# Performance work log

Measured on AMD Instinct MI355X. Metric: run time of the kernel, lower is better.

The kernel has to match this reference:

```python
import jax, jax.numpy as jnp
import numpy as np

B, N, C = 16, 2048, 80
CONF_THR = 0.2
NMS_THR = 0.45
OFFSET = 10000.0  # > max box coordinate, separates classes for batched per-class NMS


def setup_inputs() -> dict:
    key = jax.random.key(0)
    k1, k2, k3, k4 = jax.random.split(key, 4)
    cxcy = jax.random.uniform(k1, (B, N, 2)) * 640.0
    wh = jax.random.uniform(k2, (B, N, 2)) * 100.0 + 1.0
    boxes = jnp.concatenate([cxcy - wh / 2, cxcy + wh / 2], axis=-1)  # (x1,y1,x2,y2)
    scores = jax.random.uniform(k3, (B, N, 1))
    classprobs = jax.random.uniform(k4, (B, N, C))
    detection = jnp.concatenate([boxes, scores, classprobs], axis=-1)  # [B,N,85]
    return {"detection": detection}


def _iou_matrix(boxes):
    # boxes: [N,4] -> [N,N] pairwise IoU (torchvision convention, no +1)
    x1, y1, x2, y2 = boxes[:, 0], boxes[:, 1], boxes[:, 2], boxes[:, 3]
    area = jnp.clip(x2 - x1, 0.0) * jnp.clip(y2 - y1, 0.0)
    ix1 = jnp.maximum(x1[:, None], x1[None, :])
    iy1 = jnp.maximum(y1[:, None], y1[None, :])
    ix2 = jnp.minimum(x2[:, None], x2[None, :])
    iy2 = jnp.minimum(y2[:, None], y2[None, :])
    inter = jnp.clip(ix2 - ix1, 0.0) * jnp.clip(iy2 - iy1, 0.0)
    return inter / (area[:, None] + area[None, :] - inter + 1e-7)


def _filter_image(boxes, scores, classprobs, labels):
    # Confidence filter (target_class=None path)
    cand = scores > CONF_THR
    # Sort by descending score, non-candidates last (sort key is non-differentiable)
    sort_key = jnp.where(cand, scores, -jnp.inf)
    order = jnp.argsort(-jax.lax.stop_gradient(sort_key))
    b = boxes[order]
    s = scores[order]
    cp = classprobs[order]
    lb = labels[order]
    cd = cand[order]
    # Per-class NMS via coordinate offset: boxes of different classes never overlap
    ob = b + lb[:, None].astype(b.dtype) * OFFSET
    iou = _iou_matrix(ob)  # [N,N]
    idx = jnp.arange(N)

    def step(active, i):
        keep_i = active[i]
        active = active & ~(keep_i & (iou[i] > NMS_THR) & (idx > i))
        return active, keep_i

    _, keep = jax.lax.scan(step, cd, idx)
    # Final sort by descending score among kept boxes (max_predictions_per_image=-1)
    final_key = jnp.where(keep, jax.lax.stop_gradient(s), -jnp.inf)
    perm = jnp.argsort(-final_key)
    keep_p = keep[perm]
    m = keep_p.astype(b.dtype)
    out_boxes = b[perm] * m[:, None]
    out_scores = s[perm] * m
    out_classprobs = cp[perm] * m
    out_labels = jnp.where(keep_p, lb[perm], 0)
    return out_boxes, out_scores, out_classprobs, out_labels, keep_p


def reference(detection):
    # split_detections
    boxes = detection[..., :4]
    scores = detection[..., 4]
    cp_all = detection[..., 5:]
    classprobs = jnp.max(cp_all, axis=-1)
    labels = jnp.argmax(cp_all, axis=-1)
    ob, osc, ocp, olb, mask = jax.vmap(_filter_image)(boxes, scores, classprobs, labels)
    # Pack float outputs: [B, N, 6] = boxes(4) + score(1) + classprob(1); padded rows are zero
    out = jnp.concatenate([ob, osc[..., None], ocp[..., None]], axis=-1)
    return out, olb, mask
```

## Files before the change

kernel.cpp:

```cpp
#include <hip/hip_runtime.h>

#define BATCH 16
#define NBOX  2048
#define NCLS  80
#define ROWF  85
#define CONF_THRF 0.2f
#define CONF_BITS 0x3E4CCCCDu
#define NMS_THRF  0.45f
#define CAP   128
#define KCAP  128
#define JOBS  (BATCH*NCLS)

#define WS_SL   0
#define WS_CP   (WS_SL + BATCH*NBOX*8)
#define WS_KC   (WS_CP + BATCH*NBOX*4)
#define WS_KCLS (WS_KC + (size_t)JOBS*KCAP*8)

static __device__ inline unsigned long long shflx64(unsigned long long v, int m) {
  int lo = __shfl_xor((int)(unsigned)(v & 0xffffffffull), m, 64);
  int hi = __shfl_xor((int)(unsigned)(v >> 32), m, 64);
  return ((unsigned long long)(unsigned)hi << 32) | (unsigned)lo;
}

__global__ __launch_bounds__(256) void prep_kernel(const float* __restrict__ det,
                                                   unsigned long long* __restrict__ sl,
                                                   float* __restrict__ cp_ws,
                                                   float* __restrict__ outz) {
  const int tid = threadIdx.x;
  const int lane = tid & 63, wavei = tid >> 6;
  const int sub = lane & 15, grp = lane >> 4;
  const int row = blockIdx.x * 16 + wavei * 4 + grp;

  int gid = blockIdx.x * 256 + tid;
  if (gid < (BATCH * NBOX * 8) / 4)
    ((float4*)outz)[gid] = make_float4(0.f, 0.f, 0.f, 0.f);

  const float* r = det + (size_t)row * ROWF;
  float best = r[5 + sub];
  int bc = sub;
#pragma unroll
  for (int k = 1; k < 5; ++k) {
    float v = r[5 + sub + 16 * k];
    if (v > best) { best = v; bc = sub + 16 * k; }
  }
#pragma unroll
  for (int d = 1; d < 16; d <<= 1) {
    float ov = __shfl_xor(best, d, 16);
    int oc = __shfl_xor(bc, d, 16);
    if (ov > best || (ov == best && oc < bc)) { best = ov; bc = oc; }
  }
  if (sub == 0) {
    sl[row] = ((unsigned long long)__float_as_uint(r[4]) << 32) | (unsigned)bc;
    cp_ws[row] = best;
  }
}

__global__ __launch_bounds__(256) void nms16_kernel(const float* __restrict__ det,
                                                    const unsigned long long* __restrict__ sl,
                                                    unsigned long long* __restrict__ keptc,
                                                    int* __restrict__ kcls) {
  __shared__ unsigned short cand[4][CAP];
  const int tid = threadIdx.x;
  const int lane = tid & 63, wid = tid >> 6;
  const int j = blockIdx.x * 4 + wid;
  const int img = j / NCLS, c = j - img * NCLS;
  const size_t ibase = (size_t)img * NBOX;
  const unsigned long long* slImg = sl + ibase;
  unsigned short* mycand = cand[wid];

  unsigned mymask = 0;
#pragma unroll
  for (int it = 0; it < 32; ++it) {
    unsigned long long v = slImg[it * 64 + lane];
    bool match = ((unsigned)(v >> 32) > CONF_BITS) && ((unsigned)v == (unsigned)c);
    mymask |= (match ? 1u : 0u) << it;
  }
  int mycnt = __popc(mymask);
  int inc = mycnt;
#pragma unroll
  for (int d = 1; d < 64; d <<= 1) { int u = __shfl_up(inc, d, 64); if (lane >= d) inc += u; }
  int mybase = inc - mycnt;
  int total = __shfl(inc, 63, 64);
  int m = total < CAP ? total : CAP;
  {
    unsigned mk = mymask;
    int pos = mybase;
    while (mk) {
      int it = __ffs(mk) - 1; mk &= mk - 1;
      if (pos < CAP) mycand[pos] = (unsigned short)(it * 64 + lane);
      pos++;
    }
  }

  unsigned long long e0 = ~0ull, e1 = ~0ull;
  if (lane < m) {
    int n = mycand[lane];
    e0 = ((unsigned long long)(~(unsigned)(slImg[n] >> 32)) << 32) | (unsigned)n;
  }
  if (lane + 64 < m) {
    int n = mycand[lane + 64];
    e1 = ((unsigned long long)(~(unsigned)(slImg[n] >> 32)) << 32) | (unsigned)n;
  }
  const bool two = (m > 64);
  if (!two) {
#pragma unroll
    for (int k = 2; k <= 64; k <<= 1)
      for (int jj = k >> 1; jj > 0; jj >>= 1) {
        bool amLow = (lane & jj) == 0;
        bool up = ((lane & k) == 0);
        unsigned long long o = shflx64(e0, jj);
        e0 = (up == amLow) ? (e0 < o ? e0 : o) : (e0 > o ? e0 : o);
      }
  } else {
#pragma unroll
    for (int k = 2; k <= 128; k <<= 1)
      for (int jj = k >> 1; jj > 0; jj >>= 1) {
        if (jj == 64) {
          bool up = ((lane & k) == 0);
          if (up ? (e0 > e1) : (e0 < e1)) { unsigned long long t = e0; e0 = e1; e1 = t; }
        } else {
          bool amLow = (lane & jj) == 0;
          bool up0 = ((lane & k) == 0), up1 = (((lane + 64) & k) == 0);
          unsigned long long o0 = shflx64(e0, jj), o1 = shflx64(e1, jj);
          e0 = (up0 == amLow) ? (e0 < o0 ? e0 : o0) : (e0 > o0 ? e0 : o0);
          e1 = (up1 == amLow) ? (e1 < o1 ? e1 : o1) : (e1 > o1 ? e1 : o1);
        }
      }
  }

  const float off = (float)c * 10000.0f;
  bool valid0 = lane < m, valid1 = two && (lane + 64 < m);
  int n0 = (int)((unsigned)e0 & (NBOX - 1));
  int n1 = (int)((unsigned)e1 & (NBOX - 1));
  float x1 = 0, y1 = 0, x2 = 0, y2 = 0, ar = 0;
  if (valid0) {
    const float* rr = det + (ibase + n0) * ROWF;
    x1 = rr[0] + off; y1 = rr[1] + off; x2 = rr[2] + off; y2 = rr[3] + off;
    ar = fmaxf(x2 - x1, 0.0f) * fmaxf(y2 - y1, 0.0f);
  }
  float X1 = 0, Y1 = 0, X2 = 0, Y2 = 0, AR = 0;
  if (valid1) {
    const float* rr = det + (ibase + n1) * ROWF;
    X1 = rr[0] + off; Y1 = rr[1] + off; X2 = rr[2] + off; Y2 = rr[3] + off;
    AR = fmaxf(X2 - X1, 0.0f) * fmaxf(Y2 - Y1, 0.0f);
  }

  unsigned long long keptm0 = 0, und = __ballot(valid0);
  while (und) {
    int i = __ffsll((long long)und) - 1;
    keptm0 |= 1ull << i;
    float kx1 = __shfl(x1, i, 64), ky1 = __shfl(y1, i, 64);
    float kx2 = __shfl(x2, i, 64), ky2 = __shfl(y2, i, 64);
    float kar = __shfl(ar, i, 64);
    float iw = fminf(x2, kx2) - fmaxf(x1, kx1);
    float ih = fminf(y2, ky2) - fmaxf(y1, ky1);
    float inter = fmaxf(iw, 0.0f) * fmaxf(ih, 0.0f);
    float iou = inter / (((kar + ar) - inter) + 1e-7f);
    bool sup = (lane > i) && (iou > NMS_THRF);
    und &= ~__ballot(sup);
    und &= ~(1ull << i);
  }
  unsigned long long keptm1 = 0;
  if (two) {
    bool dead = false;
    unsigned long long km = keptm0;
    while (km) {
      int t = __ffsll((long long)km) - 1; km &= km - 1;
      float kx1 = __shfl(x1, t, 64), ky1 = __shfl(y1, t, 64);
      float kx2 = __shfl(x2, t, 64), ky2 = __shfl(y2, t, 64);
      float kar = __shfl(ar, t, 64);
      float iw = fminf(X2, kx2) - fmaxf(X1, kx1);
      float ih = fminf(Y2, ky2) - fmaxf(Y1, ky1);
      float inter = fmaxf(iw, 0.0f) * fmaxf(ih, 0.0f);
      float iou = inter / (((kar + AR) - inter) + 1e-7f);
      dead |= (iou > NMS_THRF);
    }
    unsigned long long und1 = __ballot(valid1 && !dead);
    while (und1) {
      int i = __ffsll((long long)und1) - 1;
      keptm1 |= 1ull << i;
      float kx1 = __shfl(X1, i, 64), ky1 = __shfl(Y1, i, 64);
      float kx2 = __shfl(X2, i, 64), ky2 = __shfl(Y2, i, 64);
      float kar = __shfl(AR, i, 64);
      float iw = fminf(X2, kx2) - fmaxf(X1, kx1);
      float ih = fminf(Y2, ky2) - fmaxf(Y1, ky1);
      float inter = fmaxf(iw, 0.0f) * fmaxf(ih, 0.0f);
      float iou = inter / (((kar + AR) - inter) + 1e-7f);
      bool sup = (lane > i) && (iou > NMS_THRF);
      und1 &= ~__ballot(sup);
      und1 &= ~(1ull << i);
    }
  }

  unsigned long long* dst = keptc + (size_t)j * KCAP;
  if ((keptm0 >> lane) & 1) {
    int rank = __popcll(keptm0 & ((1ull << lane) - 1ull));
    dst[rank] = (e0 & 0xffffffff00000000ull) | (unsigned)((n0 << 7) | c);
  }
  if (two && ((keptm1 >> lane) & 1)) {
    int rank = __popcll(keptm0) + __popcll(keptm1 & ((1ull << lane) - 1ull));
    dst[rank] = (e1 & 0xffffffff00000000ull) | (unsigned)((n1 << 7) | c);
  }
  if (lane == 0) kcls[j] = __popcll(keptm0) + __popcll(keptm1);
}

__global__ __launch_bounds__(1024) void outr_kernel(const float* __restrict__ det,
                                                    const float* __restrict__ cp_ws,
                                                    const unsigned long long* __restrict__ keptc,
                                                    const int* __restrict__ kcls,
                                                    float* __restrict__ out) {
  __shared__ unsigned long long keys[NBOX];
  __shared__ int offL[NCLS], cntL[NCLS];
  __shared__ int KtotS;
  const int img = blockIdx.x >> 5, seg = blockIdx.x & 31;
  const int tid = threadIdx.x;
  const int lane = tid & 63, wid = tid >> 6;
  const size_t ibase = (size_t)img * NBOX;

  if (wid == 0) {
    int v0 = kcls[img * NCLS + lane];
    int v1 = (lane < NCLS - 64) ? kcls[img * NCLS + 64 + lane] : 0;
    int s0 = v0;
#pragma unroll
    for (int d = 1; d < 64; d <<= 1) { int u = __shfl_up(s0, d, 64); if (lane >= d) s0 += u; }
    int total0 = __shfl(s0, 63, 64);
    int s1 = v1;
#pragma unroll
    for (int d = 1; d < 16; d <<= 1) { int u = __shfl_up(s1, d, 64); if (lane >= d) s1 += u; }
    offL[lane] = s0 - v0; cntL[lane] = v0;
    if (lane < NCLS - 64) { offL[64 + lane] = total0 + s1 - v1; cntL[64 + lane] = v1; }
    if (lane == 15) KtotS = total0 + s1;
  }
  __syncthreads();
  const int K = KtotS;
  if (seg * 64 >= K) return;

  for (int c = wid; c < NCLS; c += 16) {
    int kc = cntL[c], o = offL[c];
    const unsigned long long* src = keptc + (size_t)(img * NCLS + c) * KCAP;
    for (int q = lane; q < kc; q += 64) keys[o + q] = src[q];
  }
  __syncthreads();

  const int sbase = seg * 64 + (wid << 2);
  unsigned long long X[4];
  bool V[4];
#pragma unroll
  for (int q = 0; q < 4; ++q) {
    V[q] = (sbase + q) < K;
    X[q] = V[q] ? keys[sbase + q] : ~0ull;
  }

  const int bA = offL[lane], nA = cntL[lane];
  int bB = 0, nB = 0;
  if (lane < NCLS - 64) { bB = offL[64 + lane]; nB = cntL[64 + lane]; }
  int loA[4], hiA[4], loB[4], hiB[4];
#pragma unroll
  for (int q = 0; q < 4; ++q) {
    loA[q] = 0; hiA[q] = V[q] ? nA : 0;
    loB[q] = 0; hiB[q] = (lane < NCLS - 64 && V[q]) ? nB : 0;
  }
#pragma unroll
  for (int s = 0; s < 8; ++s) {
#pragma unroll
    for (int q = 0; q < 4; ++q) {
      if (loA[q] < hiA[q]) {
        int mid = (loA[q] + hiA[q]) >> 1;
        if (keys[bA + mid] < X[q]) loA[q] = mid + 1; else hiA[q] = mid;
      }
      if (loB[q] < hiB[q]) {
        int mid = (loB[q] + hiB[q]) >> 1;
        if (keys[bB + mid] < X[q]) loB[q] = mid + 1; else hiB[q] = mid;
      }
    }
  }
  int r[4];
#pragma unroll
  for (int q = 0; q < 4; ++q) {
    int v = loA[q] + loB[q];
#pragma unroll
    for (int d = 1; d < 64; d <<= 1) v += __shfl_xor(v, d, 64);
    r[q] = v;
  }

  if (lane < 4 && V[lane & 3]) {
    unsigned long long xm = (lane == 0) ? X[0] : (lane == 1) ? X[1] : (lane == 2) ? X[2] : X[3];
    int rm = (lane == 0) ? r[0] : (lane == 1) ? r[1] : (lane == 2) ? r[2] : r[3];
    unsigned meta = (unsigned)xm;
    int idx = (meta >> 7) & (NBOX - 1);
    int lb = meta & 127;
    const float* rr = det + (ibase + idx) * ROWF;
    float* orow = out + (ibase + rm) * 6;
    orow[0] = rr[0]; orow[1] = rr[1]; orow[2] = rr[2]; orow[3] = rr[3];
    orow[4] = __uint_as_float(~(unsigned)(xm >> 32));
    orow[5] = cp_ws[ibase + idx];
    out[(size_t)BATCH * NBOX * 6 + ibase + rm] = (float)lb;
    out[(size_t)BATCH * NBOX * 7 + ibase + rm] = 1.0f;
  }
}

extern "C" void kernel_launch(void* const* d_in, const int* in_sizes, int n_in,
                              void* d_out, int out_size, void* d_ws, size_t ws_size,
                              hipStream_t stream) {
  const float* det = (const float*)d_in[0];
  float* out = (float*)d_out;
  char* ws = (char*)d_ws;

  unsigned long long* sl = (unsigned long long*)(ws + WS_SL);
  float* cp_ws = (float*)(ws + WS_CP);
  unsigned long long* keptc = (unsigned long long*)(ws + WS_KC);
  int* kcls = (int*)(ws + WS_KCLS);

  prep_kernel<<<BATCH * NBOX / 16, 256, 0, stream>>>(det, sl, cp_ws, out);
  nms16_kernel<<<JOBS / 4, 256, 0, stream>>>(det, sl, keptc, kcls);
  outr_kernel<<<BATCH * 32, 1024, 0, stream>>>(det, cp_ws, keptc, kcls, out);
}
```

Measured before the change: 32.13 us.

## Split output ranking into gather kernel plus brute-force rank-count kernel

The final output stage is split into two kernels. One gathers each image's kept keys from the per-class lists into a contiguous padded global array. The second computes each kept box's output rank by counting smaller keys with a linear scan, one thread per box. This replaces the per-class binary searches in shared memory and the wave-wide reductions with simple uniform loads. The cost is an extra kernel launch, a global round trip, and O(K^2) comparisons per image.

```diff
diff --git a/kernel.cpp b/kernel.cpp
--- a/kernel.cpp
+++ b/kernel.cpp
@@ -15,6 +15,8 @@
 #define WS_CP   (WS_SL + BATCH*NBOX*8)
 #define WS_KC   (WS_CP + BATCH*NBOX*4)
 #define WS_KCLS (WS_KC + (size_t)JOBS*KCAP*8)
+#define WS_KD   (WS_KCLS + JOBS*4)
+#define WS_KK   (WS_KD + (size_t)BATCH*NBOX*8)
 
 static __device__ inline unsigned long long shflx64(unsigned long long v, int m) {
   int lo = __shfl_xor((int)(unsigned)(v & 0xffffffffull), m, 64);
@@ -204,18 +206,15 @@
   if (lane == 0) kcls[j] = __popcll(keptm0) + __popcll(keptm1);
 }
 
-__global__ __launch_bounds__(1024) void outr_kernel(const float* __restrict__ det,
-                                                    const float* __restrict__ cp_ws,
-                                                    const unsigned long long* __restrict__ keptc,
+__global__ __launch_bounds__(1024) void gath_kernel(const unsigned long long* __restrict__ keptc,
                                                     const int* __restrict__ kcls,
-                                                    float* __restrict__ out) {
-  __shared__ unsigned long long keys[NBOX];
+                                                    unsigned long long* __restrict__ kd,
+                                                    int* __restrict__ kK) {
   __shared__ int offL[NCLS], cntL[NCLS];
   __shared__ int KtotS;
-  const int img = blockIdx.x >> 5, seg = blockIdx.x & 31;
+  const int img = blockIdx.x;
   const int tid = threadIdx.x;
   const int lane = tid & 63, wid = tid >> 6;
-  const size_t ibase = (size_t)img * NBOX;
 
   if (wid == 0) {
     int v0 = kcls[img * NCLS + lane];
@@ -229,73 +228,59 @@
     for (int d = 1; d < 16; d <<= 1) { int u = __shfl_up(s1, d, 64); if (lane >= d) s1 += u; }
     offL[lane] = s0 - v0; cntL[lane] = v0;
     if (lane < NCLS - 64) { offL[64 + lane] = total0 + s1 - v1; cntL[64 + lane] = v1; }
-    if (lane == 15) KtotS = total0 + s1;
+    if (lane == 15) { KtotS = total0 + s1; kK[img] = total0 + s1; }
   }
   __syncthreads();
-  const int K = KtotS;
-  if (seg * 64 >= K) return;
-
+
+  unsigned long long* kimg = kd + (size_t)img * NBOX;
   for (int c = wid; c < NCLS; c += 16) {
     int kc = cntL[c], o = offL[c];
     const unsigned long long* src = keptc + (size_t)(img * NCLS + c) * KCAP;
-    for (int q = lane; q < kc; q += 64) keys[o + q] = src[q];
-  }
-  __syncthreads();
-
-  const int sbase = seg * 64 + (wid << 2);
-  unsigned long long X[4];
-  bool V[4];
-#pragma unroll
-  for (int q = 0; q < 4; ++q) {
-    V[q] = (sbase + q) < K;
-    X[q] = V[q] ? keys[sbase + q] : ~0ull;
-  }
-
-  const int bA = offL[lane], nA = cntL[lane];
-  int bB = 0, nB = 0;
-  if (lane < NCLS - 64) { bB = offL[64 + lane]; nB = cntL[64 + lane]; }
-  int loA[4], hiA[4], loB[4], hiB[4];
-#pragma unroll
-  for (int q = 0; q < 4; ++q) {
-    loA[q] = 0; hiA[q] = V[q] ? nA : 0;
-    loB[q] = 0; hiB[q] = (lane < NCLS - 64 && V[q]) ? nB : 0;
-  }
-#pragma unroll
-  for (int s = 0; s < 8; ++s) {
-#pragma unroll
-    for (int q = 0; q < 4; ++q) {
-      if (loA[q] < hiA[q]) {
-        int mid = (loA[q] + hiA[q]) >> 1;
-        if (keys[bA + mid] < X[q]) loA[q] = mid + 1; else hiA[q] = mid;
-      }
-      if (loB[q] < hiB[q]) {
-        int mid = (loB[q] + hiB[q]) >> 1;
-        if (keys[bB + mid] < X[q]) loB[q] = mid + 1; else hiB[q] = mid;
-      }
-    }
-  }
-  int r[4];
-#pragma unroll
-  for (int q = 0; q < 4; ++q) {
-    int v = loA[q] + loB[q];
-#pragma unroll
-    for (int d = 1; d < 64; d <<= 1) v += __shfl_xor(v, d, 64);
-    r[q] = v;
-  }
-
-  if (lane < 4 && V[lane & 3]) {
-    unsigned long long xm = (lane == 0) ? X[0] : (lane == 1) ? X[1] : (lane == 2) ? X[2] : X[3];
-    int rm = (lane == 0) ? r[0] : (lane == 1) ? r[1] : (lane == 2) ? r[2] : r[3];
-    unsigned meta = (unsigned)xm;
+    for (int q = lane; q < kc; q += 64) kimg[o + q] = src[q];
+  }
+  const int K = KtotS;
+  const int Kpad = (K + 63) & ~63;
+  for (int i = K + tid; i < Kpad; i += 1024) kimg[i] = ~0ull;
+}
+
+__global__ __launch_bounds__(256) void outc2_kernel(const float* __restrict__ det,
+                                                    const float* __restrict__ cp_ws,
+                                                    const unsigned long long* __restrict__ kd,
+                                                    const int* __restrict__ kK,
+                                                    float* __restrict__ out) {
+  const int img = blockIdx.x >> 3, seg = blockIdx.x & 7;
+  const int tid = threadIdx.x;
+  const int K = kK[img];
+  if (seg * 256 >= K) return;
+  const size_t ibase = (size_t)img * NBOX;
+  const unsigned long long* kimg = kd + ibase;
+
+  const int p = seg * 256 + tid;
+  const bool v = p < K;
+  unsigned long long x = v ? kimg[p] : ~0ull;
+
+  const int Kpad = (K + 63) & ~63;
+  int cnt = 0;
+  for (int t = 0; t < Kpad; t += 8) {
+    unsigned long long y0 = kimg[t + 0], y1 = kimg[t + 1];
+    unsigned long long y2 = kimg[t + 2], y3 = kimg[t + 3];
+    unsigned long long y4 = kimg[t + 4], y5 = kimg[t + 5];
+    unsigned long long y6 = kimg[t + 6], y7 = kimg[t + 7];
+    cnt += (y0 < x) + (y1 < x) + (y2 < x) + (y3 < x)
+         + (y4 < x) + (y5 < x) + (y6 < x) + (y7 < x);
+  }
+
+  if (v) {
+    unsigned meta = (unsigned)x;
     int idx = (meta >> 7) & (NBOX - 1);
     int lb = meta & 127;
     const float* rr = det + (ibase + idx) * ROWF;
-    float* orow = out + (ibase + rm) * 6;
+    float* orow = out + (ibase + cnt) * 6;
     orow[0] = rr[0]; orow[1] = rr[1]; orow[2] = rr[2]; orow[3] = rr[3];
-    orow[4] = __uint_as_float(~(unsigned)(xm >> 32));
+    orow[4] = __uint_as_float(~(unsigned)(x >> 32));
     orow[5] = cp_ws[ibase + idx];
-    out[(size_t)BATCH * NBOX * 6 + ibase + rm] = (float)lb;
-    out[(size_t)BATCH * NBOX * 7 + ibase + rm] = 1.0f;
+    out[(size_t)BATCH * NBOX * 6 + ibase + cnt] = (float)lb;
+    out[(size_t)BATCH * NBOX * 7 + ibase + cnt] = 1.0f;
   }
 }
 
@@ -310,8 +295,11 @@
   float* cp_ws = (float*)(ws + WS_CP);
   unsigned long long* keptc = (unsigned long long*)(ws + WS_KC);
   int* kcls = (int*)(ws + WS_KCLS);
+  unsigned long long* kd = (unsigned long long*)(ws + WS_KD);
+  int* kK = (int*)(ws + WS_KK);
 
   prep_kernel<<<BATCH * NBOX / 16, 256, 0, stream>>>(det, sl, cp_ws, out);
   nms16_kernel<<<JOBS / 4, 256, 0, stream>>>(det, sl, keptc, kcls);
-  outr_kernel<<<BATCH * 32, 1024, 0, stream>>>(det, cp_ws, keptc, kcls, out);
-}
+  gath_kernel<<<BATCH, 1024, 0, stream>>>(keptc, kcls, kd, kK);
+  outc2_kernel<<<BATCH * 8, 256, 0, stream>>>(det, cp_ws, kd, kK, out);
+}
```

Measured after the change: 90.31 us. 2.81x slower.
